# Kernel tuning notes

Measured on AMD Instinct MI355X. Metric: run time of the kernel, lower is better.

## Reference

```python
import jax, jax.numpy as jnp
import numpy as np

N_EMBED = 2048
N_HEAD = 16
HEAD_DIM = N_EMBED // N_HEAD
LN_EPS = 1e-5


def setup_inputs() -> dict:
    key = jax.random.key(0)
    ks = jax.random.split(key, 12)
    B, S, D = 4, 2048, N_EMBED
    s = 0.02
    inp = {
        "x": jax.random.normal(ks[0], (B, S, D), jnp.float32),
        "ln1_w": jnp.ones((D,), jnp.float32),
        "ln1_b": jnp.zeros((D,), jnp.float32),
        "Wqkv": jax.random.normal(ks[1], (3 * D, D), jnp.float32) * s,
        "bqkv": jnp.zeros((3 * D,), jnp.float32),
        "Wo": jax.random.normal(ks[2], (D, D), jnp.float32) * s,
        "bo": jnp.zeros((D,), jnp.float32),
        "ln2_w": jnp.ones((D,), jnp.float32),
        "ln2_b": jnp.zeros((D,), jnp.float32),
        "W1": jax.random.normal(ks[3], (4 * D, D), jnp.float32) * s,
        "b1": jnp.zeros((4 * D,), jnp.float32),
        "W2": jax.random.normal(ks[4], (D, 4 * D), jnp.float32) * s,
        "b2": jnp.zeros((D,), jnp.float32),
        # ALiBi slopes: 2^(-8*(h+1)/n_head)
        "slopes": jnp.asarray(2.0 ** (-8.0 * (np.arange(1, N_HEAD + 1)) / N_HEAD), jnp.float32),
    }
    return inp


def layer_norm(x, w, b):
    mu = jnp.mean(x, axis=-1, keepdims=True)
    var = jnp.mean(jnp.square(x - mu), axis=-1, keepdims=True)
    return (x - mu) * jax.lax.rsqrt(var + LN_EPS) * w + b


def attention(h, Wqkv, bqkv, Wo, bo, slopes):
    B, S, D = h.shape
    qkv = jnp.einsum("bsd,ed->bse", h, Wqkv) + bqkv  # [B,S,3D]
    q, k, v = jnp.split(qkv, 3, axis=-1)
    q = q.reshape(B, S, N_HEAD, HEAD_DIM).transpose(0, 2, 1, 3)
    k = k.reshape(B, S, N_HEAD, HEAD_DIM).transpose(0, 2, 1, 3)
    v = v.reshape(B, S, N_HEAD, HEAD_DIM).transpose(0, 2, 1, 3)
    scores = jnp.einsum("bhqd,bhkd->bhqk", q, k) / jnp.sqrt(jnp.float32(HEAD_DIM))
    pos = jnp.arange(S)
    rel = pos[None, :] - pos[:, None]  # j - i, <= 0 on causal part
    alibi = slopes[:, None, None] * rel[None, :, :].astype(jnp.float32)  # [H,S,S]
    causal = rel <= 0
    scores = jnp.where(causal[None, None], scores + alibi[None], -jnp.inf)
    attn = jax.nn.softmax(scores, axis=-1)
    out = jnp.einsum("bhqk,bhkd->bhqd", attn, v)
    out = out.transpose(0, 2, 1, 3).reshape(B, S, D)
    return jnp.einsum("bsd,ed->bse", out, Wo) + bo


def reference(x, ln1_w, ln1_b, Wqkv, bqkv, Wo, bo, ln2_w, ln2_b, W1, b1, W2, b2, slopes):
    # Pre-LN block; dropout in eval mode (identity)
    x = x + attention(layer_norm(x, ln1_w, ln1_b), Wqkv, bqkv, Wo, bo, slopes)
    h = layer_norm(x, ln2_w, ln2_b)
    h = jax.nn.gelu(jnp.einsum("bsd,fd->bsf", h, W1) + b1, approximate=False)
    x = x + jnp.einsum("bsf,df->bsd", h, W2) + b2
    return x
```

## Files before the change

### kernel.cpp

```cpp
#include <hip/hip_runtime.h>

typedef unsigned short ushort_t;
typedef __attribute__((ext_vector_type(8))) short short8;
typedef __attribute__((ext_vector_type(4))) float floatx4;
typedef __attribute__((ext_vector_type(4))) unsigned short ush4;

#define MFMA16x16x32(a, b, c) __builtin_amdgcn_mfma_f32_16x16x32_bf16(a, b, c, 0, 0, 0)

__device__ __forceinline__ float bf2f(ushort_t h) {
    unsigned int u = ((unsigned int)h) << 16;
    return __builtin_bit_cast(float, u);
}
__device__ __forceinline__ ushort_t f2bf(float f) {
    unsigned int u = __builtin_bit_cast(unsigned int, f);
    u += 0x7fffu + ((u >> 16) & 1u);
    return (ushort_t)(u >> 16);
}
__device__ __forceinline__ void gload_lds16(const ushort_t* g, ushort_t* l) {
    __builtin_amdgcn_global_load_lds(
        (const __attribute__((address_space(1))) unsigned int*)g,
        (__attribute__((address_space(3))) unsigned int*)l, 16, 0, 0);
}

__global__ __launch_bounds__(256) void conv_bf16(const float* __restrict__ in,
                                                 ushort_t* __restrict__ out, int n8) {
    int i = blockIdx.x * 256 + threadIdx.x;
    const int stride = gridDim.x * 256;
    for (; i < n8; i += stride) {
        const float* p = in + (size_t)i * 8;
        floatx4 a0 = *(const floatx4*)p;
        floatx4 a1 = *(const floatx4*)(p + 4);
        short8 o;
        o[0] = (short)f2bf(a0[0]); o[1] = (short)f2bf(a0[1]);
        o[2] = (short)f2bf(a0[2]); o[3] = (short)f2bf(a0[3]);
        o[4] = (short)f2bf(a1[0]); o[5] = (short)f2bf(a1[1]);
        o[6] = (short)f2bf(a1[2]); o[7] = (short)f2bf(a1[3]);
        *(short8*)(out + (size_t)i * 8) = o;
    }
}

template <int INF32>
__global__ __launch_bounds__(256) void ln_kernel(const void* __restrict__ in,
                                                 const ushort_t* __restrict__ w,
                                                 const ushort_t* __restrict__ b,
                                                 ushort_t* __restrict__ out) {
    const int row = blockIdx.x;
    const int tid = threadIdx.x;
    const size_t base = (size_t)row * 2048 + (size_t)tid * 8;
    float v[8];
    if (INF32) {
        const float* p = (const float*)in + base;
        floatx4 a0 = *(const floatx4*)p;
        floatx4 a1 = *(const floatx4*)(p + 4);
        v[0] = a0[0]; v[1] = a0[1]; v[2] = a0[2]; v[3] = a0[3];
        v[4] = a1[0]; v[5] = a1[1]; v[6] = a1[2]; v[7] = a1[3];
    } else {
        short8 hv = *(const short8*)((const ushort_t*)in + base);
        const ushort_t* hp = (const ushort_t*)&hv;
#pragma unroll
        for (int k = 0; k < 8; k++) v[k] = bf2f(hp[k]);
    }
    float s = 0.f, sq = 0.f;
#pragma unroll
    for (int k = 0; k < 8; k++) { s += v[k]; sq += v[k] * v[k]; }
#pragma unroll
    for (int m = 32; m; m >>= 1) { s += __shfl_xor(s, m); sq += __shfl_xor(sq, m); }
    __shared__ float red[8];
    const int wv = tid >> 6;
    if ((tid & 63) == 0) { red[wv] = s; red[4 + wv] = sq; }
    __syncthreads();
    s = red[0] + red[1] + red[2] + red[3];
    sq = red[4] + red[5] + red[6] + red[7];
    const float mu = s * (1.f / 2048.f);
    const float var = fmaxf(sq * (1.f / 2048.f) - mu * mu, 0.f);
    const float rs = rsqrtf(var + 1e-5f);
    short8 ov;
#pragma unroll
    for (int k = 0; k < 8; k++) {
        const int c = tid * 8 + k;
        float y = (v[k] - mu) * rs * bf2f(w[c]) + bf2f(b[c]);
        ov[k] = (short)f2bf(y);
    }
    *(short8*)(out + base) = ov;
}

template <int EPI>
__global__ __launch_bounds__(512, 2) void gemm256(const ushort_t* __restrict__ A,
                                                  const ushort_t* __restrict__ W,
                                                  const ushort_t* __restrict__ bias,
                                                  const void* __restrict__ res,
                                                  void* __restrict__ out,
                                                  int M, int N, int K) {
    __shared__ ushort_t smem[65536];
    ushort_t* const As0 = smem;
    ushort_t* const Bs0 = smem + 16384;
    ushort_t* const As1 = smem + 32768;
    ushort_t* const Bs1 = smem + 49152;
    const int tid = threadIdx.x;
    const int lane = tid & 63;
    const int wave = tid >> 6;
    const int la = lane & 15;
    const int qd = lane >> 4;
    const int wrow = (wave >> 2) * 128;
    const int wcol = (wave & 3) * 64;
    const int nbn = N >> 8;
    int bm, bn;
    {
        int wg = (int)blockIdx.x;
        const int cpx = (int)gridDim.x >> 3;
        wg = (wg & 7) * cpx + (wg >> 3);
        const int per = 8 * nbn;
        const int g = wg / per;
        const int rem = wg - g * per;
        bm = g * 8 + (rem & 7);
        bn = rem >> 3;
    }
    const int srow = tid >> 3;
    const int schunk = (tid & 7) ^ (srow & 7);
    const ushort_t* gA = A + (size_t)(bm * 256 + srow) * K + schunk * 8;
    const ushort_t* gB = W + (size_t)(bn * 256 + srow) * K + schunk * 8;
    const int wbase = (tid & ~63) * 8;

    floatx4 acc[8][4];
    const floatx4 z4 = {0.f, 0.f, 0.f, 0.f};
#pragma unroll
    for (int i = 0; i < 8; i++)
#pragma unroll
        for (int j = 0; j < 4; j++) acc[i][j] = z4;
    short8 a[4][2], b[4][2];

#define GBAR()                                    \
    do {                                          \
        asm volatile("" ::: "memory");            \
        __builtin_amdgcn_s_barrier();             \
        asm volatile("" ::: "memory");            \
    } while (0)
#define GLGKM0() asm volatile("s_waitcnt lgkmcnt(0)" ::: "memory")
#define GVM4() asm volatile("s_waitcnt vmcnt(4)" ::: "memory")
#define STG(gp, lb, h, koff)                                                               \
    do {                                                                                   \
        gload_lds16((gp) + (size_t)((h) * 128) * K + (koff), (lb) + ((h) * 128) * 64 + wbase); \
        gload_lds16((gp) + (size_t)((h) * 128 + 64) * K + (koff),                          \
                    (lb) + ((h) * 128 + 64) * 64 + wbase);                                 \
    } while (0)
#define LDA4(base, mh)                                                                     \
    do {                                                                                   \
        _Pragma("unroll") for (int mi = 0; mi < 4; mi++) {                                 \
            const int row_ = wrow + (mh) * 64 + mi * 16 + la;                              \
            a[mi][0] = *(const short8*)&(base)[row_ * 64 + ((qd ^ (la & 7)) * 8)];         \
            a[mi][1] = *(const short8*)&(base)[row_ * 64 + (((4 | qd) ^ (la & 7)) * 8)];   \
        }                                                                                  \
    } while (0)
#define LDB2(base, nl)                                                                     \
    do {                                                                                   \
        _Pragma("unroll") for (int nj = 0; nj < 2; nj++) {                                 \
            const int row_ = wcol + ((nl) + nj) * 16 + la;                                 \
            b[(nl) + nj][0] = *(const short8*)&(base)[row_ * 64 + ((qd ^ (la & 7)) * 8)];  \
            b[(nl) + nj][1] =                                                              \
                *(const short8*)&(base)[row_ * 64 + (((4 | qd) ^ (la & 7)) * 8)];          \
        }                                                                                  \
    } while (0)
#define MMQ(mb, nl)                                                                        \
    do {                                                                                   \
        _Pragma("unroll") for (int ks = 0; ks < 2; ks++)                                   \
            _Pragma("unroll") for (int mi = 0; mi < 4; mi++)                               \
                _Pragma("unroll") for (int nj = 0; nj < 2; nj++) acc[(mb) + mi][(nl) + nj] = \
                    MFMA16x16x32(a[mi][ks], b[(nl) + nj][ks], acc[(mb) + mi][(nl) + nj]);  \
    } while (0)

    const int NT = K >> 6;
    STG(gB, Bs0, 0, 0); STG(gB, Bs0, 1, 0);
    STG(gA, As0, 0, 0); STG(gA, As0, 1, 0);
    STG(gB, Bs1, 0, 64); STG(gB, Bs1, 1, 64);
    GVM4(); GBAR();

    for (int t = 0; t < NT; t += 2) {
        const size_t kA1 = (size_t)(t + 1) * 64;
        const size_t kT2 = (size_t)((t + 2 < NT) ? t + 2 : NT - 1) * 64;
        const size_t kB3 = (size_t)((t + 3 < NT) ? t + 3 : NT - 1) * 64;
        LDA4(As0, 0); LDB2(Bs0, 0); STG(gA, As1, 0, kA1);
        GBAR(); GLGKM0();
        __builtin_amdgcn_s_setprio(1); MMQ(0, 0); __builtin_amdgcn_s_setprio(0);
        GBAR();
        LDB2(Bs0, 2); STG(gA, As1, 1, kA1);
        GBAR(); GLGKM0();
        __builtin_amdgcn_s_setprio(1); MMQ(0, 2); __builtin_amdgcn_s_setprio(0);
        GBAR();
        LDA4(As0, 1); STG(gB, Bs0, 0, kT2);
        GBAR(); GLGKM0();
        __builtin_amdgcn_s_setprio(1); MMQ(4, 2); __builtin_amdgcn_s_setprio(0);
        GBAR();
        STG(gB, Bs0, 1, kT2);
        GBAR();
        __builtin_amdgcn_s_setprio(1); MMQ(4, 0); __builtin_amdgcn_s_setprio(0);
        GVM4(); GBAR();
        LDA4(As1, 0); LDB2(Bs1, 0); STG(gA, As0, 0, kT2);
        GBAR(); GLGKM0();
        __builtin_amdgcn_s_setprio(1); MMQ(0, 0); __builtin_amdgcn_s_setprio(0);
        GBAR();
        LDB2(Bs1, 2); STG(gA, As0, 1, kT2);
        GBAR(); GLGKM0();
        __builtin_amdgcn_s_setprio(1); MMQ(0, 2); __builtin_amdgcn_s_setprio(0);
        GBAR();
        LDA4(As1, 1); STG(gB, Bs1, 0, kB3);
        GBAR(); GLGKM0();
        __builtin_amdgcn_s_setprio(1); MMQ(4, 2); __builtin_amdgcn_s_setprio(0);
        GBAR();
        STG(gB, Bs1, 1, kB3);
        GBAR();
        __builtin_amdgcn_s_setprio(1); MMQ(4, 0); __builtin_amdgcn_s_setprio(0);
        GVM4(); GBAR();
    }
#undef GBAR
#undef GLGKM0
#undef GVM4
#undef STG
#undef LDA4
#undef LDB2
#undef MMQ

    if (EPI == 0) {
        ushort_t* q_out = (ushort_t*)out;
        if (bn < 16) {
            const float qs = (bn < 8) ? 0.08838834764831845f : 1.0f;
            ushort_t* dst = (bn < 8) ? q_out : (q_out + 16777216);
#pragma unroll
            for (int i = 0; i < 8; i++)
#pragma unroll
                for (int j = 0; j < 4; j++)
#pragma unroll
                    for (int r = 0; r < 4; r++) {
                        const int m = bm * 256 + wrow + i * 16 + qd * 4 + r;
                        const int n = bn * 256 + wcol + j * 16 + la;
                        dst[(size_t)m * 2048 + (n & 2047)] =
                            f2bf((acc[i][j][r] + bf2f(bias[n])) * qs);
                    }
        } else {
            ushort_t* v_out = q_out + 33554432;
#pragma unroll
            for (int i = 0; i < 8; i++)
#pragma unroll
                for (int j = 0; j < 4; j++) {
                    const int n = bn * 256 + wcol + j * 16 + la;
                    const int d = n - 4096;
                    const int m0 = bm * 256 + wrow + i * 16 + qd * 4;
                    const int bb = m0 >> 11, s = m0 & 2047;
                    const float bv = bf2f(bias[n]);
                    ush4 pk;
#pragma unroll
                    for (int r = 0; r < 4; r++) pk[r] = f2bf(acc[i][j][r] + bv);
                    *(ush4*)&v_out[((size_t)(bb * 2048 + d)) * 2048 + s] = pk;
                }
        }
    } else {
#pragma unroll
        for (int i = 0; i < 8; i++)
#pragma unroll
            for (int j = 0; j < 4; j++)
#pragma unroll
                for (int r = 0; r < 4; r++) {
                    const int m = bm * 256 + wrow + i * 16 + qd * 4 + r;
                    const int n = bn * 256 + wcol + j * 16 + la;
                    const size_t idx = (size_t)m * N + n;
                    float v = acc[i][j][r] + bf2f(bias[n]);
                    if (EPI == 1) {
                        v += ((const float*)res)[idx];
                        ((ushort_t*)out)[idx] = f2bf(v);
                    } else if (EPI == 2) {
                        v = 0.5f * v * (1.f + erff(v * 0.70710678118654752f));
                        ((ushort_t*)out)[idx] = f2bf(v);
                    } else {
                        v += bf2f(((const ushort_t*)res)[idx]);
                        ((float*)out)[idx] = v;
                    }
                }
    }
}

__global__ __launch_bounds__(256, 4) void attn_kernel(const ushort_t* __restrict__ qb,
                                                      const ushort_t* __restrict__ kb,
                                                      const ushort_t* __restrict__ vtb,
                                                      const float* __restrict__ slopes,
                                                      ushort_t* __restrict__ out) {
    __shared__ ushort_t Ks[8192];
    __shared__ ushort_t Vt[8192];
    __shared__ ushort_t Ps[4096];
    const int tid = threadIdx.x;
    const int lane = tid & 63;
    const int wave = tid >> 6;
    const int la = lane & 15;
    const int qd = lane >> 4;
    const int qt = blockIdx.x;
    const int h = blockIdx.y;
    const int b = blockIdx.z;
    const float slope = slopes[h];

    const size_t qrow = (size_t)(b * 2048 + qt * 64 + wave * 16 + la);
    short8 qa[4];
#pragma unroll
    for (int ks = 0; ks < 4; ks++)
        qa[ks] = *(const short8*)&qb[qrow * 2048 + h * 128 + (ks * 4 + qd) * 8];

    const ushort_t* kbase = kb + ((size_t)b * 2048) * 2048 + h * 128;
    const ushort_t* vbase = vtb + ((size_t)(b * 2048 + h * 128)) * 2048;

    floatx4 accO[8];
    const floatx4 z4 = {0.f, 0.f, 0.f, 0.f};
#pragma unroll
    for (int dt = 0; dt < 8; dt++) accO[dt] = z4;
    float mst[4] = {-1e30f, -1e30f, -1e30f, -1e30f};
    float lst[4] = {0.f, 0.f, 0.f, 0.f};

    for (int kt = 0; kt <= qt; kt++) {
        __syncthreads();
#pragma unroll
        for (int p = 0; p < 4; p++) {
            const int f = p * 256 + tid;
            const int r = f >> 4;
            const int cs = f & 15;
            gload_lds16(kbase + (size_t)(kt * 64 + r) * 2048 + (cs ^ (r & 15)) * 8,
                        Ks + (size_t)(p * 256 + (tid & ~63)) * 8);
        }
#pragma unroll
        for (int p = 0; p < 4; p++) {
            const int f = p * 256 + tid;
            const int d = f >> 3;
            const int c = f & 7;
            gload_lds16(vbase + (size_t)d * 2048 + kt * 64 + (c ^ (d & 7)) * 8,
                        Vt + (size_t)(p * 256 + (tid & ~63)) * 8);
        }
        __syncthreads();

        floatx4 sc[4];
#pragma unroll
        for (int nt = 0; nt < 4; nt++) sc[nt] = z4;
#pragma unroll
        for (int nt = 0; nt < 4; nt++) {
#pragma unroll
            for (int ks = 0; ks < 4; ks++) {
                short8 kf = *(const short8*)&Ks[(nt * 16 + la) * 128 + ((ks * 4 + qd) ^ la) * 8];
                sc[nt] = MFMA16x16x32(qa[ks], kf, sc[nt]);
            }
        }

        const int knb = kt * 64;
        const bool diag = (kt == qt);
        ushort_t* Pw = Ps + wave * 1024;
#pragma unroll
        for (int r = 0; r < 4; r++) {
            float rmax = -1e30f;
#pragma unroll
            for (int nt = 0; nt < 4; nt++) {
                float sval = sc[nt][r] + slope * (float)(knb + nt * 16 + la);
                if (diag && (nt * 16 + la > wave * 16 + qd * 4 + r)) sval = -1e30f;
                sc[nt][r] = sval;
                rmax = fmaxf(rmax, sval);
            }
            rmax = fmaxf(rmax, __shfl_xor(rmax, 1));
            rmax = fmaxf(rmax, __shfl_xor(rmax, 2));
            rmax = fmaxf(rmax, __shfl_xor(rmax, 4));
            rmax = fmaxf(rmax, __shfl_xor(rmax, 8));
            const float mnew = fmaxf(mst[r], rmax);
            const int row = qd * 4 + r;
            float rsum = 0.f;
#pragma unroll
            for (int nt = 0; nt < 4; nt++) {
                const float pv = __expf(sc[nt][r] - mnew);
                rsum += pv;
                const int col = nt * 16 + la;
                Pw[row * 64 + ((col >> 3) ^ (row & 7)) * 8 + (col & 7)] = f2bf(pv);
            }
            rsum += __shfl_xor(rsum, 1);
            rsum += __shfl_xor(rsum, 2);
            rsum += __shfl_xor(rsum, 4);
            rsum += __shfl_xor(rsum, 8);
            const float alpha = __expf(mst[r] - mnew);
            mst[r] = mnew;
            lst[r] = lst[r] * alpha + rsum;
#pragma unroll
            for (int dt = 0; dt < 8; dt++) accO[dt][r] *= alpha;
        }

#pragma unroll
        for (int k2 = 0; k2 < 2; k2++) {
            short8 pa = *(const short8*)&Pw[la * 64 + ((k2 * 4 + qd) ^ (la & 7)) * 8];
#pragma unroll
            for (int dt = 0; dt < 8; dt++) {
                const int d = dt * 16 + la;
                short8 vf = *(const short8*)&Vt[d * 64 + ((k2 * 4 + qd) ^ (d & 7)) * 8];
                accO[dt] = MFMA16x16x32(pa, vf, accO[dt]);
            }
        }
    }

    const size_t orow0 = (size_t)b * 2048 + qt * 64 + wave * 16 + qd * 4;
#pragma unroll
    for (int r = 0; r < 4; r++) {
        const float inv = 1.f / lst[r];
#pragma unroll
        for (int dt = 0; dt < 8; dt++)
            out[(orow0 + r) * 2048 + h * 128 + dt * 16 + la] = f2bf(accO[dt][r] * inv);
    }
}

extern "C" void kernel_launch(void* const* d_in, const int* in_sizes, int n_in,
                              void* d_out, int out_size, void* d_ws, size_t ws_size,
                              hipStream_t stream) {
    (void)in_sizes; (void)n_in; (void)out_size; (void)ws_size;
    const float* x      = (const float*)d_in[0];
    const float* ln1w   = (const float*)d_in[1];
    const float* ln1b   = (const float*)d_in[2];
    const float* Wqkv   = (const float*)d_in[3];
    const float* bqkv   = (const float*)d_in[4];
    const float* Wo     = (const float*)d_in[5];
    const float* bo     = (const float*)d_in[6];
    const float* ln2w   = (const float*)d_in[7];
    const float* ln2b   = (const float*)d_in[8];
    const float* W1     = (const float*)d_in[9];
    const float* b1     = (const float*)d_in[10];
    const float* W2     = (const float*)d_in[11];
    const float* b2     = (const float*)d_in[12];
    const float* slopes = (const float*)d_in[13];
    float* outp = (float*)d_out;

    char* ws = (char*)d_ws;
    const size_t MB = 1ull << 20;
    ushort_t* wbuf  = (ushort_t*)(ws);
    ushort_t* sv    = (ushort_t*)(ws + 36 * MB);
    ushort_t* ln1w_c = sv;
    ushort_t* ln1b_c = sv + 2048;
    ushort_t* bqkv_c = sv + 4096;
    ushort_t* bo_c   = sv + 10240;
    ushort_t* ln2w_c = sv + 12288;
    ushort_t* ln2b_c = sv + 14336;
    ushort_t* b1_c   = sv + 16384;
    ushort_t* b2_c   = sv + 24576;
    ushort_t* h_buf    = (ushort_t*)(ws + 37 * MB);
    ushort_t* q_buf    = (ushort_t*)(ws + 69 * MB);
    ushort_t* k_buf    = (ushort_t*)(ws + 101 * MB);
    ushort_t* vt_buf   = (ushort_t*)(ws + 133 * MB);
    ushort_t* attn_buf = (ushort_t*)(ws + 165 * MB);
    ushort_t* act_buf  = q_buf;
    ushort_t* x2_buf   = (ushort_t*)(ws + 197 * MB);

    const int M = 8192;

    conv_bf16<<<8, 256, 0, stream>>>(ln1w, ln1w_c, 2048 / 8);
    conv_bf16<<<8, 256, 0, stream>>>(ln1b, ln1b_c, 2048 / 8);
    ln_kernel<1><<<M, 256, 0, stream>>>(x, ln1w_c, ln1b_c, h_buf);
    conv_bf16<<<2048, 256, 0, stream>>>(Wqkv, wbuf, (6144 * 2048) / 8);
    conv_bf16<<<8, 256, 0, stream>>>(bqkv, bqkv_c, 6144 / 8);
    gemm256<0><<<(M / 256) * (6144 / 256), 512, 0, stream>>>(
        h_buf, wbuf, bqkv_c, nullptr, q_buf, M, 6144, 2048);
    attn_kernel<<<dim3(32, 16, 4), 256, 0, stream>>>(q_buf, k_buf, vt_buf, slopes, attn_buf);
    conv_bf16<<<1024, 256, 0, stream>>>(Wo, wbuf, (2048 * 2048) / 8);
    conv_bf16<<<8, 256, 0, stream>>>(bo, bo_c, 2048 / 8);
    gemm256<1><<<(M / 256) * (2048 / 256), 512, 0, stream>>>(
        attn_buf, wbuf, bo_c, x, x2_buf, M, 2048, 2048);
    conv_bf16<<<8, 256, 0, stream>>>(ln2w, ln2w_c, 2048 / 8);
    conv_bf16<<<8, 256, 0, stream>>>(ln2b, ln2b_c, 2048 / 8);
    ln_kernel<0><<<M, 256, 0, stream>>>(x2_buf, ln2w_c, ln2b_c, h_buf);
    conv_bf16<<<2048, 256, 0, stream>>>(W1, wbuf, (8192 * 2048) / 8);
    conv_bf16<<<8, 256, 0, stream>>>(b1, b1_c, 8192 / 8);
    gemm256<2><<<(M / 256) * (8192 / 256), 512, 0, stream>>>(
        h_buf, wbuf, b1_c, nullptr, act_buf, M, 8192, 2048);
    conv_bf16<<<2048, 256, 0, stream>>>(W2, wbuf, (2048 * 8192) / 8);
    conv_bf16<<<8, 256, 0, stream>>>(b2, b2_c, 2048 / 8);
    gemm256<3><<<(M / 256) * (2048 / 256), 512, 0, stream>>>(
        act_buf, wbuf, b2_c, x2_buf, outp, M, 2048, 8192);
}
```

Before: 1.374 ms.

## Double-buffer K/V tiles in attention, reorder blocks longest-first, use exp2 softmax

```diff
diff --git a/kernel.cpp b/kernel.cpp
--- a/kernel.cpp
+++ b/kernel.cpp
@@ -222,7 +222,7 @@
     if (EPI == 0) {
         ushort_t* q_out = (ushort_t*)out;
         if (bn < 16) {
-            const float qs = (bn < 8) ? 0.08838834764831845f : 1.0f;
+            const float qs = (bn < 8) ? (0.08838834764831845f * 1.4426950408889634f) : 1.0f;
             ushort_t* dst = (bn < 8) ? q_out : (q_out + 16777216);
 #pragma unroll
             for (int i = 0; i < 8; i++)
@@ -277,23 +277,25 @@
     }
 }
 
-__global__ __launch_bounds__(256, 4) void attn_kernel(const ushort_t* __restrict__ qb,
+__global__ __launch_bounds__(256, 2) void attn_kernel(const ushort_t* __restrict__ qb,
                                                       const ushort_t* __restrict__ kb,
                                                       const ushort_t* __restrict__ vtb,
                                                       const float* __restrict__ slopes,
                                                       ushort_t* __restrict__ out) {
-    __shared__ ushort_t Ks[8192];
-    __shared__ ushort_t Vt[8192];
+    __shared__ ushort_t Ks[16384];
+    __shared__ ushort_t Vt[16384];
     __shared__ ushort_t Ps[4096];
     const int tid = threadIdx.x;
     const int lane = tid & 63;
     const int wave = tid >> 6;
     const int la = lane & 15;
     const int qd = lane >> 4;
-    const int qt = blockIdx.x;
-    const int h = blockIdx.y;
-    const int b = blockIdx.z;
-    const float slope = slopes[h];
+    const int lid = (int)blockIdx.x;
+    const int pair = (lid & 7) * 8 + (lid >> 8);
+    const int h = pair & 15;
+    const int b = pair >> 4;
+    const int qt = 31 - ((lid >> 3) & 31);
+    const float slope2 = slopes[h] * 1.4426950408889634f;
 
     const size_t qrow = (size_t)(b * 2048 + qt * 64 + wave * 16 + la);
     short8 qa[4];
@@ -311,25 +313,42 @@
     float mst[4] = {-1e30f, -1e30f, -1e30f, -1e30f};
     float lst[4] = {0.f, 0.f, 0.f, 0.f};
 
+#define AISSUE(kt_, buf_)                                                                   \
+    do {                                                                                    \
+        _Pragma("unroll") for (int p_ = 0; p_ < 4; p_++) {                                  \
+            const int f_ = p_ * 256 + tid;                                                  \
+            const int r_ = f_ >> 4;                                                         \
+            const int cs_ = f_ & 15;                                                        \
+            gload_lds16(kbase + (size_t)((kt_) * 64 + r_) * 2048 + (cs_ ^ (r_ & 15)) * 8,   \
+                        Ks + (buf_) * 8192 + (size_t)(p_ * 256 + (tid & ~63)) * 8);         \
+        }                                                                                   \
+        _Pragma("unroll") for (int p_ = 0; p_ < 4; p_++) {                                  \
+            const int f_ = p_ * 256 + tid;                                                  \
+            const int d_ = f_ >> 3;                                                         \
+            const int c_ = f_ & 7;                                                          \
+            gload_lds16(vbase + (size_t)d_ * 2048 + (kt_) * 64 + (c_ ^ (d_ & 7)) * 8,       \
+                        Vt + (buf_) * 8192 + (size_t)(p_ * 256 + (tid & ~63)) * 8);         \
+        }                                                                                   \
+    } while (0)
+#define ABAR()                                    \
+    do {                                          \
+        asm volatile("" ::: "memory");            \
+        __builtin_amdgcn_s_barrier();             \
+        asm volatile("" ::: "memory");            \
+    } while (0)
+
+    AISSUE(0, 0);
     for (int kt = 0; kt <= qt; kt++) {
-        __syncthreads();
-#pragma unroll
-        for (int p = 0; p < 4; p++) {
-            const int f = p * 256 + tid;
-            const int r = f >> 4;
-            const int cs = f & 15;
-            gload_lds16(kbase + (size_t)(kt * 64 + r) * 2048 + (cs ^ (r & 15)) * 8,
-                        Ks + (size_t)(p * 256 + (tid & ~63)) * 8);
+        const int cur = kt & 1;
+        if (kt < qt) {
+            AISSUE(kt + 1, cur ^ 1);
+            asm volatile("s_waitcnt vmcnt(8)" ::: "memory");
+        } else {
+            asm volatile("s_waitcnt vmcnt(0)" ::: "memory");
         }
-#pragma unroll
-        for (int p = 0; p < 4; p++) {
-            const int f = p * 256 + tid;
-            const int d = f >> 3;
-            const int c = f & 7;
-            gload_lds16(vbase + (size_t)d * 2048 + kt * 64 + (c ^ (d & 7)) * 8,
-                        Vt + (size_t)(p * 256 + (tid & ~63)) * 8);
-        }
-        __syncthreads();
+        ABAR();
+        const ushort_t* Kc = Ks + cur * 8192;
+        const ushort_t* Vc = Vt + cur * 8192;
 
         floatx4 sc[4];
 #pragma unroll
@@ -338,7 +357,7 @@
         for (int nt = 0; nt < 4; nt++) {
 #pragma unroll
             for (int ks = 0; ks < 4; ks++) {
-                short8 kf = *(const short8*)&Ks[(nt * 16 + la) * 128 + ((ks * 4 + qd) ^ la) * 8];
+                short8 kf = *(const short8*)&Kc[(nt * 16 + la) * 128 + ((ks * 4 + qd) ^ la) * 8];
                 sc[nt] = MFMA16x16x32(qa[ks], kf, sc[nt]);
             }
         }
@@ -346,12 +365,16 @@
         const int knb = kt * 64;
         const bool diag = (kt == qt);
         ushort_t* Pw = Ps + wave * 1024;
+        float acol[4];
+#pragma unroll
+        for (int nt = 0; nt < 4; nt++)
+            acol[nt] = slope2 * (float)(knb + nt * 16 + la);
 #pragma unroll
         for (int r = 0; r < 4; r++) {
             float rmax = -1e30f;
 #pragma unroll
             for (int nt = 0; nt < 4; nt++) {
-                float sval = sc[nt][r] + slope * (float)(knb + nt * 16 + la);
+                float sval = sc[nt][r] + acol[nt];
                 if (diag && (nt * 16 + la > wave * 16 + qd * 4 + r)) sval = -1e30f;
                 sc[nt][r] = sval;
                 rmax = fmaxf(rmax, sval);
@@ -365,7 +388,7 @@
             float rsum = 0.f;
 #pragma unroll
             for (int nt = 0; nt < 4; nt++) {
-                const float pv = __expf(sc[nt][r] - mnew);
+                const float pv = __builtin_amdgcn_exp2f(sc[nt][r] - mnew);
                 rsum += pv;
                 const int col = nt * 16 + la;
                 Pw[row * 64 + ((col >> 3) ^ (row & 7)) * 8 + (col & 7)] = f2bf(pv);
@@ -374,7 +397,7 @@
             rsum += __shfl_xor(rsum, 2);
             rsum += __shfl_xor(rsum, 4);
             rsum += __shfl_xor(rsum, 8);
-            const float alpha = __expf(mst[r] - mnew);
+            const float alpha = __builtin_amdgcn_exp2f(mst[r] - mnew);
             mst[r] = mnew;
             lst[r] = lst[r] * alpha + rsum;
 #pragma unroll
@@ -387,11 +410,14 @@
 #pragma unroll
             for (int dt = 0; dt < 8; dt++) {
                 const int d = dt * 16 + la;
-                short8 vf = *(const short8*)&Vt[d * 64 + ((k2 * 4 + qd) ^ (d & 7)) * 8];
+                short8 vf = *(const short8*)&Vc[d * 64 + ((k2 * 4 + qd) ^ (d & 7)) * 8];
                 accO[dt] = MFMA16x16x32(pa, vf, accO[dt]);
             }
         }
-    }
+        ABAR();
+    }
+#undef AISSUE
+#undef ABAR
 
     const size_t orow0 = (size_t)b * 2048 + qt * 64 + wave * 16 + qd * 4;
 #pragma unroll
@@ -452,7 +478,7 @@
     conv_bf16<<<8, 256, 0, stream>>>(bqkv, bqkv_c, 6144 / 8);
     gemm256<0><<<(M / 256) * (6144 / 256), 512, 0, stream>>>(
         h_buf, wbuf, bqkv_c, nullptr, q_buf, M, 6144, 2048);
-    attn_kernel<<<dim3(32, 16, 4), 256, 0, stream>>>(q_buf, k_buf, vt_buf, slopes, attn_buf);
+    attn_kernel<<<2048, 256, 0, stream>>>(q_buf, k_buf, vt_buf, slopes, attn_buf);
     conv_bf16<<<1024, 256, 0, stream>>>(Wo, wbuf, (2048 * 2048) / 8);
     conv_bf16<<<8, 256, 0, stream>>>(bo, bo_c, 2048 / 8);
     gemm256<1><<<(M / 256) * (2048 / 256), 512, 0, stream>>>(
```

Measured after the change: 1.252 ms. 1.1x faster.
